# Kernel tuning notes

Measured on AMD Instinct MI355X. Metric: run time of the kernel, lower is better.

The kernel has to match this reference:

```python
import jax, jax.numpy as jnp
import numpy as np

B, N, PLANE, H, W = 2, 6, 64, 48, 48
HIDP = 64
PS = 3
RATES = 3


def conv2d(x, w, b, pad, dil=1):
    # x: [BN, Cin, H, W], w: [Cout, Cin, kh, kw]
    out = jax.lax.conv_general_dilated(
        x, w, window_strides=(1, 1),
        padding=[(pad, pad), (pad, pad)],
        rhs_dilation=(dil, dil),
        dimension_numbers=('NCHW', 'OIHW', 'NCHW'))
    return out + b[None, :, None, None]


def avgpool3(x):
    bn, c, h, w = x.shape
    return x.reshape(bn, c, h // PS, PS, w // PS, PS).mean(axis=(3, 5))


def setup_inputs() -> dict:
    key = jax.random.key(0)
    ks = jax.random.split(key, 20)
    s = 0.05
    hid_pa = PLANE * 3  # 192, hidden width of MultiFieldConv2d
    d = {
        'x': jax.random.normal(ks[0], (B, N, PLANE, H, W), jnp.float32),
        # patch_aggr: 3 dilated convs (rates 1..3), k=3, plane -> plane*3
        'pa_w1': jax.random.normal(ks[1], (hid_pa, PLANE, 3, 3)) * s,
        'pa_b1': jnp.zeros((hid_pa,)),
        'pa_w2': jax.random.normal(ks[2], (hid_pa, PLANE, 3, 3)) * s,
        'pa_b2': jnp.zeros((hid_pa,)),
        'pa_w3': jax.random.normal(ks[3], (hid_pa, PLANE, 3, 3)) * s,
        'pa_b3': jnp.zeros((hid_pa,)),
        # convert: 1x1 (hid_pa*rates -> 3*hidp), relu, 1x1 (3*hidp -> 3*hidp)
        'pa_cw1': jax.random.normal(ks[4], (3 * HIDP, hid_pa * RATES, 1, 1)) * s,
        'pa_cb1': jnp.zeros((3 * HIDP,)),
        'pa_cw2': jax.random.normal(ks[5], (3 * HIDP, 3 * HIDP, 1, 1)) * s,
        'pa_cb2': jnp.zeros((3 * HIDP,)),
        # to_kv conv: k=3 pad=1, hidp -> hidp
        'kv_w': jax.random.normal(ks[6], (HIDP, HIDP, 3, 3)) * s,
        'kv_b': jnp.zeros((HIDP,)),
        # to_out: 1x1 hidp->plane, relu, 1x1 plane->plane, relu
        'out_w1': jax.random.normal(ks[7], (PLANE, HIDP, 1, 1)) * s,
        'out_b1': jnp.zeros((PLANE,)),
        'out_w2': jax.random.normal(ks[8], (PLANE, PLANE, 1, 1)) * s,
        'out_b2': jnp.zeros((PLANE,)),
        'scales': jnp.ones((N,)),
    }
    return d


def reference(x, pa_w1, pa_b1, pa_w2, pa_b2, pa_w3, pa_b3,
              pa_cw1, pa_cb1, pa_cw2, pa_cb2,
              kv_w, kv_b, out_w1, out_b1, out_w2, out_b2, scales):
    b, n, c, h, w = x.shape
    scale = HIDP ** (-0.5)
    xf = x.reshape(b * n, c, h, w)

    # MultiFieldConv2d: dilated convs (same spatial size for odd k), concat, 1x1 convert
    u = jnp.concatenate([
        conv2d(xf, pa_w1, pa_b1, pad=1, dil=1),
        conv2d(xf, pa_w2, pa_b2, pad=2, dil=2),
        conv2d(xf, pa_w3, pa_b3, pad=3, dil=3),
    ], axis=1)
    qkv = conv2d(jax.nn.relu(conv2d(u, pa_cw1, pa_cb1, 0)), pa_cw2, pa_cb2, 0)
    qkv = jax.nn.relu(qkv)  # F.relu(patch_aggr(x))
    xq, xk, xv = jnp.split(qkv, 3, axis=1)  # each [BN, hidp, H, W]

    def to_kv(t):
        return avgpool3(jax.nn.relu(conv2d(t, kv_w, kv_b, pad=PS // 2)))

    k_ = to_kv(xk)                       # [BN, hidp, H/3, W/3]
    v_ = to_kv(xv) * (1.0 / PS ** 2)

    hw_kv = k_.shape[2] * k_.shape[3]
    Qs = xq.reshape(b, n, HIDP, h * w).transpose(0, 1, 3, 2)   # b n g d
    Ks = k_.reshape(b, n, HIDP, hw_kv).transpose(0, 1, 3, 2)   # b m k d
    Vs = v_.reshape(b, n, HIDP, hw_kv).transpose(0, 1, 3, 2)

    # Leave-one-out sigmoid attention: sum_{j != i} sigmoid(q_i k_j^T * scale) @ v_j
    # Computed as full sum minus the self (j == i) term (exact same math).
    A_all = jax.nn.sigmoid(jnp.einsum('bngd,bmkd->bngmk', Qs, Ks) * scale)
    out_all = jnp.einsum('bngmk,bmkd->bngd', A_all, Vs)
    A_self = jax.nn.sigmoid(jnp.einsum('bngd,bnkd->bngk', Qs, Ks) * scale)
    out_self = jnp.einsum('bngk,bnkd->bngd', A_self, Vs)
    attn_out = out_all - out_self                               # [b, n, HW, hidp]

    res = attn_out.transpose(0, 1, 3, 2).reshape(b, n, HIDP, h, w)
    xv5 = xv.reshape(b, n, HIDP, h, w)
    res = jax.nn.relu(res + scales[None, :, None, None, None] * xv5)

    rf = res.reshape(b * n, HIDP, h, w)
    o = jax.nn.relu(conv2d(jax.nn.relu(conv2d(rf, out_w1, out_b1, 0)), out_w2, out_b2, 0))
    return o.reshape(b, n, c, h, w)
```

## Files before the change

kernel.cpp:

```cpp
#include <hip/hip_runtime.h>
#include <hip/hip_bf16.h>
#include <math.h>

#define BB 2
#define NVIEW 6
#define BN 12
#define CIN 64
#define HH 48
#define WW 48
#define PP (HH*WW)
#define OC 192
#define HPA 192
#define HIDP 64
#define KHW 16
#define PK 256
#define PADW 54
#define PADA (PADW*PADW)
#define NTOT (BN*PP)
#define K1 1728
#define KVPW 50
#define KVPA (KVPW*KVPW)

typedef __attribute__((ext_vector_type(8))) short bf16x8;
typedef __attribute__((ext_vector_type(4))) float f32x4;

#define OFF_WEFFB 0
#define SZ_WEFFB_FL (OC*K1/2)
#define OFF_BEFF (OFF_WEFFB + SZ_WEFFB_FL)
#define SZ_BEFF 256
#define OFF_CW2B (OFF_BEFF + SZ_BEFF)
#define SZ_CW2B_FL (OC*OC/2)
#define OFF_WKVB (OFF_CW2B + SZ_CW2B_FL)
#define SZ_WKVB_FL (64*576/2)
#define OFF_PADXT (OFF_WKVB + SZ_WKVB_FL)
#define SZ_PADXT_FL (BN*PADA*64/2)
#define OFF_QB16 (OFF_PADXT + SZ_PADXT_FL)
#define SZ_QB16_FL (BN*PP*64/2)
#define OFF_KB16 (OFF_QB16 + SZ_QB16_FL)
#define SZ_KB16_FL (BN*PK*64/2)
#define OFF_VB16T (OFF_KB16 + SZ_KB16_FL)
#define SZ_VB16T_FL (BN*64*PK/2)
#define OFF_KVPAD (OFF_VB16T + SZ_VB16T_FL)
#define SZ_KVPAD_FL (BN*2*KVPA*64/2)
#define OFF_CONVB (OFF_KVPAD + SZ_KVPAD_FL)
#define SZ_CONVB_FL (BN*2*PP*64/2)
#define OFF_W1SW (OFF_CONVB + SZ_CONVB_FL)
#define SZ_WSW_FL 2048
#define OFF_W2SW (OFF_W1SW + SZ_WSW_FL)
#define OFF_ATTNP (OFF_W2SW + SZ_WSW_FL)
#define SZ_ATTNP (BN*PP*HIDP)
#define OFF_XVB16 (OFF_ATTNP + 2*SZ_ATTNP)
#define SZ_XVB16_FL (BN*PP*64/2)

__device__ __forceinline__ void load_lds16(const void* g, void* l) {
    __builtin_amdgcn_global_load_lds(
        (const __attribute__((address_space(1))) unsigned int*)g,
        (__attribute__((address_space(3))) unsigned int*)l, 16, 0, 0);
}

__device__ __forceinline__ unsigned short f2bu(float f) {
    __hip_bfloat16 h = __float2bfloat16(f);
    return *(unsigned short*)&h;
}

__device__ __forceinline__ float bu2f(unsigned short h) {
    unsigned int u = ((unsigned int)h) << 16;
    return *(float*)&u;
}

__global__ __launch_bounds__(192) void k_fold(const float* __restrict__ cw1,
                       const float* __restrict__ cb1,
                       const float* __restrict__ w1, const float* __restrict__ b1,
                       const float* __restrict__ w2, const float* __restrict__ b2,
                       const float* __restrict__ w3, const float* __restrict__ b3,
                       __hip_bfloat16* __restrict__ weffb, float* __restrict__ beff) {
    __shared__ float cw1s[8][HPA];
    int b = blockIdx.x;
    int r = b / 72;
    int rem = b % 72;
    int og = rem / 3, tz = rem % 3;
    int tid = threadIdx.x;
    int tg = tz*192 + tid;
    int ic = tg / 9, tap = tg % 9;
    const float* w = (r==0) ? w1 : (r==1) ? w2 : w3;
    #pragma unroll
    for (int j = 0; j < 8; ++j)
        cw1s[j][tid] = cw1[(size_t)(og*8+j)*(HPA*3) + r*HPA + tid];
    __syncthreads();
    float acc[8] = {0,0,0,0,0,0,0,0};
    for (int c = 0; c < HPA; ++c) {
        float wv = w[(size_t)c*(CIN*9) + tg];
        #pragma unroll
        for (int j = 0; j < 8; ++j)
            acc[j] += cw1s[j][c] * wv;
    }
    #pragma unroll
    for (int j = 0; j < 8; ++j)
        weffb[(size_t)(og*8+j)*K1 + r*576 + tap*64 + ic] = __float2bfloat16(acc[j]);
    if (r == 0 && tz == 0 && tid < 8) {
        int o = og*8 + tid;
        float bacc = cb1[o];
        for (int rr = 0; rr < 3; ++rr) {
            const float* bb = (rr==0)?b1:(rr==1)?b2:b3;
            for (int c = 0; c < HPA; ++c)
                bacc += cw1[(size_t)o*(HPA*3) + rr*HPA + c] * bb[c];
        }
        beff[o] = bacc;
    }
}

__global__ void k_wprep(const float* __restrict__ kvw, const float* __restrict__ cw2,
                        const float* __restrict__ w1, const float* __restrict__ w2,
                        __hip_bfloat16* __restrict__ wkvb, __hip_bfloat16* __restrict__ cw2b,
                        __hip_bfloat16* __restrict__ w1sw, __hip_bfloat16* __restrict__ w2sw) {
    int idx = blockIdx.x*256 + threadIdx.x;
    if (idx < 36864) {
        int oc = idx / 576, rest = idx % 576;
        int tap = rest / 64, ic = rest % 64;
        wkvb[idx] = __float2bfloat16(kvw[(oc*64 + ic)*9 + tap]);
    } else if (idx < 73728) {
        int i = idx - 36864;
        cw2b[i] = __float2bfloat16(cw2[i]);
    } else if (idx < 81920) {
        int i = idx - 73728;
        const float* w = (i < 4096) ? w1 : w2;
        __hip_bfloat16* dst = (i < 4096) ? w1sw : w2sw;
        int j = i & 4095;
        int oc = j >> 6, s = (j >> 3) & 7, e = j & 7;
        int k = ((s ^ (oc & 7)) << 3) + e;
        dst[j] = __float2bfloat16(w[oc*64 + k]);
    }
}

__global__ void k_padxT(const float* __restrict__ x, __hip_bfloat16* __restrict__ padxT) {
    int idx = blockIdx.x*256 + threadIdx.x;
    if (idx >= BN*PADA) return;
    int spos = idx % PADA; int bn = idx / PADA;
    int sy = spos / PADW, sx = spos % PADW;
    __hip_bfloat16* dst = padxT + (size_t)idx*64;
    if (sy >= 3 && sy < 51 && sx >= 3 && sx < 51) {
        const float* src = x + (size_t)bn*CIN*PP + (sy-3)*WW + (sx-3);
        #pragma unroll 8
        for (int ic = 0; ic < 64; ++ic) dst[ic] = __float2bfloat16(src[ic*PP]);
    } else {
        #pragma unroll 8
        for (int ic = 0; ic < 64; ++ic) dst[ic] = __float2bfloat16(0.f);
    }
}

__global__ void k_halo(__hip_bfloat16* __restrict__ kvpad) {
    int idx = blockIdx.x*256 + threadIdx.x;
    if (idx >= 24*196) return;
    int bn2 = idx / 196, h = idx % 196;
    int py, px;
    if (h < 50)       { py = 0;        px = h; }
    else if (h < 100) { py = 49;       px = h - 50; }
    else if (h < 148) { py = h - 99;   px = 0; }
    else              { py = h - 147;  px = 49; }
    bf16x8 z = (bf16x8){0,0,0,0,0,0,0,0};
    __hip_bfloat16* dst = kvpad + ((size_t)bn2*KVPA + py*KVPW + px)*64;
    #pragma unroll
    for (int j = 0; j < 8; ++j) *(bf16x8*)(dst + j*8) = z;
}

__global__ __launch_bounds__(256) void k_mfc(const __hip_bfloat16* __restrict__ wA,
        const __hip_bfloat16* __restrict__ pxT, const __hip_bfloat16* __restrict__ cw2b,
        const float* __restrict__ beff, const float* __restrict__ cb2,
        __hip_bfloat16* __restrict__ xvb16, __hip_bfloat16* __restrict__ qb16,
        __hip_bfloat16* __restrict__ kvpad) {
    __shared__ __align__(16) char smem[41472];
    int tid = threadIdx.x;
    int wid = tid >> 6, lane = tid & 63;
    int bn = blockIdx.x / 36;
    int pb = (blockIdx.x % 36) * 64;
    int sgr = ((lane&7) ^ (lane>>3)) * 8;
    int l7 = lane & 7, lh = lane >> 4, rrow = lane & 15, gcol = lane >> 4;

    size_t gbase[8];
    #pragma unroll
    for (int s2 = 0; s2 < 8; ++s2) {
        int seg = wid*8 + s2;
        if (seg < 24) {
            int row = seg*8 + (lane>>3);
            gbase[s2] = (size_t)row*K1 + sgr;
        } else {
            int p = pb + (seg-24)*8 + (lane>>3);
            int py = p / WW, px = p % WW;
            gbase[s2] = ((size_t)bn*PADA + (py+3)*PADW + (px+3))*64 + sgr;
        }
    }

    f32x4 acc1[3][4];
    #pragma unroll
    for (int m = 0; m < 3; ++m)
        #pragma unroll
        for (int nf = 0; nf < 4; ++nf) acc1[m][nf] = (f32x4){0.f,0.f,0.f,0.f};

    for (int kt = 0; kt < 27; ++kt) {
        int r_ = kt / 9, tap = kt - r_*9;
        int doff = (r_+1)*((tap/3 - 1)*PADW + (tap%3 - 1));
        __syncthreads();
        #pragma unroll
        for (int s2 = 0; s2 < 8; ++s2) {
            int seg = wid*8 + s2;
            const __hip_bfloat16* g = (seg < 24) ? wA + gbase[s2] + kt*64
                                                 : pxT + gbase[s2] + (size_t)doff*64;
            load_lds16(g, smem + seg*1024);
        }
        __syncthreads();
        bf16x8 a[3][2], b[4][2];
        #pragma unroll
        for (int kk = 0; kk < 2; ++kk) {
            int gof = ((kk*4 + lh) ^ l7) << 4;
            #pragma unroll
            for (int m = 0; m < 3; ++m)
                a[m][kk] = *(const bf16x8*)(smem + (wid*48 + m*16 + rrow)*128 + gof);
            #pragma unroll
            for (int nf = 0; nf < 4; ++nf)
                b[nf][kk] = *(const bf16x8*)(smem + 24576 + (nf*16 + rrow)*128 + gof);
        }
        #pragma unroll
        for (int kk = 0; kk < 2; ++kk)
            #pragma unroll
            for (int m = 0; m < 3; ++m)
                #pragma unroll
                for (int nf = 0; nf < 4; ++nf)
                    acc1[m][nf] = __builtin_amdgcn_mfma_f32_16x16x32_bf16(
                        a[m][kk], b[nf][kk], acc1[m][nf], 0, 0, 0);
    }

    f32x4 acc2[3][4];
    #pragma unroll
    for (int m = 0; m < 3; ++m)
        #pragma unroll
        for (int nf = 0; nf < 4; ++nf) acc2[m][nf] = (f32x4){0.f,0.f,0.f,0.f};

    for (int kt2 = 0; kt2 < 3; ++kt2) {
        __syncthreads();
        #pragma unroll
        for (int s2 = 0; s2 < 6; ++s2) {
            int seg = wid*6 + s2;
            int row = seg*8 + (lane>>3);
            load_lds16(cw2b + (size_t)row*OC + kt2*64 + sgr, smem + seg*1024);
        }
        #pragma unroll
        for (int m = 0; m < 3; ++m) {
            int oc16 = wid*48 + m*16;
            if ((oc16 >> 6) == kt2) {
                int oc0 = oc16 + gcol*4;
                float4 bz = *(const float4*)&beff[oc0];
                int cb = (oc0 - kt2*64)*2;
                #pragma unroll
                for (int nf = 0; nf < 4; ++nf) {
                    int px = nf*16 + rrow;
                    ushort4 hv;
                    hv.x = f2bu(fmaxf(acc1[m][nf][0] + bz.x, 0.f));
                    hv.y = f2bu(fmaxf(acc1[m][nf][1] + bz.y, 0.f));
                    hv.z = f2bu(fmaxf(acc1[m][nf][2] + bz.z, 0.f));
                    hv.w = f2bu(fmaxf(acc1[m][nf][3] + bz.w, 0.f));
                    *(ushort4*)(smem + 32768 + px*136 + cb) = hv;
                }
            }
        }
        __syncthreads();
        #pragma unroll
        for (int kk = 0; kk < 2; ++kk) {
            int gofA = ((kk*4 + lh) ^ l7) << 4;
            int gofB = (kk*4 + lh) << 4;
            bf16x8 a2[3], b2[4];
            #pragma unroll
            for (int m2 = 0; m2 < 3; ++m2)
                a2[m2] = *(const bf16x8*)(smem + (wid*48 + m2*16 + rrow)*128 + gofA);
            #pragma unroll
            for (int nf = 0; nf < 4; ++nf)
                b2[nf] = *(const bf16x8*)(smem + 32768 + (nf*16 + rrow)*136 + gofB);
            #pragma unroll
            for (int m2 = 0; m2 < 3; ++m2)
                #pragma unroll
                for (int nf = 0; nf < 4; ++nf)
                    acc2[m2][nf] = __builtin_amdgcn_mfma_f32_16x16x32_bf16(
                        a2[m2], b2[nf], acc2[m2][nf], 0, 0, 0);
        }
    }

    #pragma unroll
    for (int m2 = 0; m2 < 3; ++m2) {
        int oc16 = wid*48 + m2*16;
        int sec = oc16 >> 6;
        int oc0 = oc16 + gcol*4;
        float4 cz = *(const float4*)&cb2[oc0];
        #pragma unroll
        for (int nf = 0; nf < 4; ++nf) {
            int px = nf*16 + rrow;
            int p = pb + px;
            ushort4 bv;
            bv.x = f2bu(fmaxf(acc2[m2][nf][0] + cz.x, 0.f));
            bv.y = f2bu(fmaxf(acc2[m2][nf][1] + cz.y, 0.f));
            bv.z = f2bu(fmaxf(acc2[m2][nf][2] + cz.z, 0.f));
            bv.w = f2bu(fmaxf(acc2[m2][nf][3] + cz.w, 0.f));
            if (sec == 0) {
                *(ushort4*)&qb16[((size_t)bn*PP + p)*64 + oc0] = bv;
            } else {
                int kv = sec - 1;
                int py = p / WW, pxx = p % WW;
                int d = oc0 - (sec << 6);
                *(ushort4*)&kvpad[((size_t)(bn*2+kv)*KVPA + (py+1)*KVPW + pxx+1)*64 + d] = bv;
                if (kv == 1)
                    *(ushort4*)&xvb16[((size_t)bn*PP + p)*64 + d] = bv;
            }
        }
    }
}

__global__ __launch_bounds__(256) void k_kvgemm(const __hip_bfloat16* __restrict__ wA,
        const __hip_bfloat16* __restrict__ kvpad, const float* __restrict__ kvb,
        __hip_bfloat16* __restrict__ convb) {
    __shared__ __align__(16) char smem[24576];
    int tid = threadIdx.x;
    int wid = tid >> 6, lane = tid & 63;
    int tileN = blockIdx.x * 128;
    int bn2 = tileN / PP, p0 = tileN % PP;
    int sgr = ((lane&7) ^ (lane>>3)) * 8;

    size_t gbase[6];
    #pragma unroll
    for (int s2 = 0; s2 < 6; ++s2) {
        int seg = wid*6 + s2;
        if (seg < 8) {
            int row = seg*8 + (lane>>3);
            gbase[s2] = (size_t)row*576 + sgr;
        } else {
            int p = p0 + (seg-8)*8 + (lane>>3);
            int py = p / WW, px = p % WW;
            gbase[s2] = ((size_t)bn2*KVPA + (py+1)*KVPW + px+1)*64 + sgr;
        }
    }
    int wr = wid >> 1, wc = wid & 1;
    int l7 = lane & 7, lh = lane >> 4;
    int arowb[2], browb[4];
    #pragma unroll
    for (int m = 0; m < 2; ++m)
        arowb[m] = (wr*32 + m*16 + (lane&15))*128;
    #pragma unroll
    for (int nf = 0; nf < 4; ++nf)
        browb[nf] = 8192 + (wc*64 + nf*16 + (lane&15))*128;

    f32x4 acc[2][4];
    #pragma unroll
    for (int m = 0; m < 2; ++m)
        #pragma unroll
        for (int nf = 0; nf < 4; ++nf) acc[m][nf] = (f32x4){0.f,0.f,0.f,0.f};

    for (int kt = 0; kt < 9; ++kt) {
        int dy = kt/3 - 1, dx = kt%3 - 1;
        int doff = dy*KVPW + dx;
        __syncthreads();
        #pragma unroll
        for (int s2 = 0; s2 < 6; ++s2) {
            int seg = wid*6 + s2;
            const __hip_bfloat16* g = (seg < 8) ? wA + gbase[s2] + kt*64
                                                : kvpad + gbase[s2] + (size_t)doff*64;
            load_lds16(g, smem + seg*1024);
        }
        __syncthreads();
        bf16x8 a[2][2], b[4][2];
        #pragma unroll
        for (int kk = 0; kk < 2; ++kk) {
            int gof = ((kk*4 + lh) ^ l7) << 4;
            #pragma unroll
            for (int m = 0; m < 2; ++m)
                a[m][kk] = *(const bf16x8*)(smem + arowb[m] + gof);
            #pragma unroll
            for (int nf = 0; nf < 4; ++nf)
                b[nf][kk] = *(const bf16x8*)(smem + browb[nf] + gof);
        }
        #pragma unroll
        for (int kk = 0; kk < 2; ++kk)
            #pragma unroll
            for (int m = 0; m < 2; ++m)
                #pragma unroll
                for (int nf = 0; nf < 4; ++nf)
                    acc[m][nf] = __builtin_amdgcn_mfma_f32_16x16x32_bf16(
                        a[m][kk], b[nf][kk], acc[m][nf], 0, 0, 0);
    }
    #pragma unroll
    for (int m = 0; m < 2; ++m) {
        int rbase = wr*32 + m*16 + (lane>>4)*4;
        float4 bz = *(const float4*)&kvb[rbase];
        #pragma unroll
        for (int nf = 0; nf < 4; ++nf) {
            int col = p0 + wc*64 + nf*16 + (lane&15);
            ushort4 cv;
            cv.x = f2bu(fmaxf(acc[m][nf][0] + bz.x, 0.f));
            cv.y = f2bu(fmaxf(acc[m][nf][1] + bz.y, 0.f));
            cv.z = f2bu(fmaxf(acc[m][nf][2] + bz.z, 0.f));
            cv.w = f2bu(fmaxf(acc[m][nf][3] + bz.w, 0.f));
            *(ushort4*)&convb[((size_t)bn2*PP + col)*64 + rbase] = cv;
        }
    }
}

__global__ __launch_bounds__(256) void k_pool(const __hip_bfloat16* __restrict__ convb,
        __hip_bfloat16* __restrict__ kbufb, __hip_bfloat16* __restrict__ vbufT) {
    int idx = blockIdx.x*256 + threadIdx.x;
    int dg = idx % 8; idx /= 8;
    int pp = idx % PK; idx /= PK;
    int bn2 = idx;
    int kv = bn2 & 1, bn = bn2 >> 1;
    int qy = pp / KHW, qx = pp % KHW;
    float s[8] = {0,0,0,0,0,0,0,0};
    const __hip_bfloat16* base = convb + (size_t)bn2*PP*64 + dg*8;
    #pragma unroll
    for (int sy = 0; sy < 3; ++sy)
        #pragma unroll
        for (int sx = 0; sx < 3; ++sx) {
            union { bf16x8 v; unsigned short h[8]; } c;
            c.v = *(const bf16x8*)(base + ((size_t)(qy*3+sy)*WW + qx*3+sx)*64);
            #pragma unroll
            for (int j = 0; j < 8; ++j) s[j] += bu2f(c.h[j]);
        }
    if (kv == 0) {
        union { ushort4 u[2]; unsigned short h[8]; } cv;
        #pragma unroll
        for (int j = 0; j < 8; ++j) cv.h[j] = f2bu(s[j] * (1.f/9.f));
        ushort4* dst = (ushort4*)(kbufb + ((size_t)bn*PK + pp)*64 + dg*8);
        dst[0] = cv.u[0]; dst[1] = cv.u[1];
    } else {
        #pragma unroll
        for (int j = 0; j < 8; ++j)
            vbufT[((size_t)bn*64 + dg*8 + j)*PK + pp] = __float2bfloat16(s[j]*(1.f/81.f));
    }
}

__global__ __launch_bounds__(256) void k_attn3(const __hip_bfloat16* __restrict__ qb16,
        const __hip_bfloat16* __restrict__ kbufb, const __hip_bfloat16* __restrict__ vbufT,
        float* __restrict__ attnp) {
    __shared__ __align__(16) char smem[32768];
    char* Qs = smem;
    char* Ks = smem + 8192;
    char* Vs = smem + 16384;
    char* Ps = smem + 24576;
    int tid = threadIdx.x;
    int wid = tid >> 6, lane = tid & 63;
    int bid = blockIdx.x;
    int ks = bid & 1; bid >>= 1;
    int qt = bid % 36; int bn = bid / 36;
    int b = bn / NVIEW, n = bn % NVIEW;
    int p0 = qt*64;

    {
        const char* gq = (const char*)(qb16 + ((size_t)bn*PP + p0)*64);
        #pragma unroll
        for (int i = 0; i < 2; ++i) {
            int s = wid*2 + i;
            int lin = s*1024 + lane*16;
            int r = lin >> 7, c = (lin >> 4) & 7;
            int gof = (r<<7) + ((c ^ (r&7)) << 4);
            load_lds16(gq + gof, Qs + s*1024);
        }
    }
    int arow = wid*16 + (lane&15);
    int brow = lane&15;
    int gcol = lane>>4;
    int vrow = tid >> 2;
    int vc2 = (tid & 3) * 2;

    f32x4 oacc[4];
    #pragma unroll
    for (int i = 0; i < 4; ++i) oacc[i] = (f32x4){0,0,0,0};

    for (int mi = 0; mi < NVIEW-1; ++mi) {
        int m = mi + (mi >= n ? 1 : 0);
        int bnk = b*NVIEW + m;
        const char* gk = (const char*)(kbufb + (size_t)bnk*PK*64);
        const __hip_bfloat16* gv = vbufT + (size_t)bnk*64*PK;
        for (int kc = ks*2; kc < ks*2+2; ++kc) {
            __syncthreads();
            #pragma unroll
            for (int i = 0; i < 2; ++i) {
                int s = wid*2 + i;
                int lin = s*1024 + lane*16;
                int r = lin >> 7, c = (lin >> 4) & 7;
                int gof = (r<<7) + ((c ^ (r&7)) << 4);
                load_lds16(gk + (size_t)kc*8192 + gof, Ks + s*1024);
            }
            {
                const __hip_bfloat16* src = gv + vrow*PK + kc*64 + vc2*8;
                bf16x8 v0 = *(const bf16x8*)src;
                bf16x8 v1 = *(const bf16x8*)(src+8);
                *(bf16x8*)(Vs + vrow*128 + ((vc2 ^ (vrow&7))<<4)) = v0;
                *(bf16x8*)(Vs + vrow*128 + (((vc2+1) ^ (vrow&7))<<4)) = v1;
            }
            __syncthreads();
            f32x4 sacc[4];
            #pragma unroll
            for (int i = 0; i < 4; ++i) sacc[i] = (f32x4){0,0,0,0};
            #pragma unroll
            for (int kk = 0; kk < 2; ++kk) {
                int g = kk*4 + gcol;
                bf16x8 af = *(const bf16x8*)(Ks + arow*128 + ((g ^ (arow&7))<<4));
                #pragma unroll
                for (int nf = 0; nf < 4; ++nf) {
                    int q = nf*16 + brow;
                    bf16x8 bq = *(const bf16x8*)(Qs + q*128 + ((g ^ (q&7))<<4));
                    sacc[nf] = __builtin_amdgcn_mfma_f32_16x16x32_bf16(af, bq, sacc[nf], 0,0,0);
                }
            }
            {
                int kbase = wid*16 + gcol*4;
                #pragma unroll
                for (int nf = 0; nf < 4; ++nf) {
                    int q = nf*16 + brow;
                    ushort4 pu;
                    float e0 = __expf(-sacc[nf][0]*0.125f);
                    float e1 = __expf(-sacc[nf][1]*0.125f);
                    float e2 = __expf(-sacc[nf][2]*0.125f);
                    float e3 = __expf(-sacc[nf][3]*0.125f);
                    pu.x = f2bu(__builtin_amdgcn_rcpf(1.f+e0));
                    pu.y = f2bu(__builtin_amdgcn_rcpf(1.f+e1));
                    pu.z = f2bu(__builtin_amdgcn_rcpf(1.f+e2));
                    pu.w = f2bu(__builtin_amdgcn_rcpf(1.f+e3));
                    *(ushort4*)(Ps + q*128 + (((kbase>>3) ^ (q&7))<<4) + (kbase&7)*2) = pu;
                }
            }
            __syncthreads();
            #pragma unroll
            for (int kk = 0; kk < 2; ++kk) {
                int g = kk*4 + gcol;
                int qr = wid*16 + brow;
                bf16x8 pf = *(const bf16x8*)(Ps + qr*128 + ((g ^ (qr&7))<<4));
                #pragma unroll
                for (int nf = 0; nf < 4; ++nf) {
                    int d = nf*16 + brow;
                    bf16x8 vf = *(const bf16x8*)(Vs + d*128 + ((g ^ (d&7))<<4));
                    oacc[nf] = __builtin_amdgcn_mfma_f32_16x16x32_bf16(pf, vf, oacc[nf], 0,0,0);
                }
            }
        }
    }
    float* ab = attnp + (size_t)ks*SZ_ATTNP + ((size_t)bn*PP + p0)*64;
    #pragma unroll
    for (int nf = 0; nf < 4; ++nf) {
        #pragma unroll
        for (int r = 0; r < 4; ++r) {
            int q = wid*16 + gcol*4 + r;
            int d = nf*16 + brow;
            ab[(size_t)q*64 + d] = oacc[nf][r];
        }
    }
}

__global__ __launch_bounds__(256) void k_out2(const float* __restrict__ attnp,
        const __hip_bfloat16* __restrict__ xvb16, const float* __restrict__ scales,
        const __hip_bfloat16* __restrict__ w1sw, const __hip_bfloat16* __restrict__ w2sw,
        const float* __restrict__ b1, const float* __restrict__ b2,
        float* __restrict__ out) {
    __shared__ __align__(16) char smem[49152];
    char* W1s = smem;
    char* W2s = smem + 8192;
    char* Rs  = smem + 16384;
    char* Ts  = smem + 32768;
    int tid = threadIdx.x;
    int wid = tid >> 6, lane = tid & 63;
    int pix0 = blockIdx.x * 128;
    int bn = pix0 / PP;
    int pb = pix0 - bn*PP;
    float sc = scales[bn % NVIEW];

    #pragma unroll
    for (int i = 0; i < 4; ++i) {
        int seg = wid*4 + i;
        const char* src = (seg < 8) ? (const char*)w1sw + seg*1024
                                    : (const char*)w2sw + (seg-8)*1024;
        load_lds16(src + lane*16, smem + seg*1024);
    }
    {
        int p = tid >> 1, d0 = (tid & 1) * 32;
        int P = pix0 + p;
        const float* a0 = attnp + (size_t)P*64 + d0;
        const float* a1 = a0 + SZ_ATTNP;
        const __hip_bfloat16* xv = xvb16 + (size_t)P*64 + d0;
        #pragma unroll
        for (int j = 0; j < 4; ++j) {
            float4 u0 = *(const float4*)(a0 + j*8);
            float4 u1 = *(const float4*)(a0 + j*8 + 4);
            float4 v0 = *(const float4*)(a1 + j*8);
            float4 v1 = *(const float4*)(a1 + j*8 + 4);
            union { bf16x8 v; unsigned short h[8]; } xu;
            xu.v = *(const bf16x8*)(xv + j*8);
            union { bf16x8 v; unsigned short h[8]; } rv;
            rv.h[0] = f2bu(fmaxf(u0.x + v0.x + sc*bu2f(xu.h[0]), 0.f));
            rv.h[1] = f2bu(fmaxf(u0.y + v0.y + sc*bu2f(xu.h[1]), 0.f));
            rv.h[2] = f2bu(fmaxf(u0.z + v0.z + sc*bu2f(xu.h[2]), 0.f));
            rv.h[3] = f2bu(fmaxf(u0.w + v0.w + sc*bu2f(xu.h[3]), 0.f));
            rv.h[4] = f2bu(fmaxf(u1.x + v1.x + sc*bu2f(xu.h[4]), 0.f));
            rv.h[5] = f2bu(fmaxf(u1.y + v1.y + sc*bu2f(xu.h[5]), 0.f));
            rv.h[6] = f2bu(fmaxf(u1.z + v1.z + sc*bu2f(xu.h[6]), 0.f));
            rv.h[7] = f2bu(fmaxf(u1.w + v1.w + sc*bu2f(xu.h[7]), 0.f));
            int g = (d0 >> 3) + j;
            *(bf16x8*)(Rs + p*128 + ((g ^ (p&7)) << 4)) = rv.v;
        }
    }
    __syncthreads();

    int wr = wid >> 1, wc = wid & 1;
    int rrow = lane & 15, gcol = lane >> 4;
    f32x4 acc1[2][4];
    #pragma unroll
    for (int m = 0; m < 2; ++m)
        #pragma unroll
        for (int nf = 0; nf < 4; ++nf) acc1[m][nf] = (f32x4){0,0,0,0};
    #pragma unroll
    for (int kk = 0; kk < 2; ++kk) {
        int g = kk*4 + gcol;
        #pragma unroll
        for (int m = 0; m < 2; ++m) {
            int oc = wr*32 + m*16 + rrow;
            bf16x8 af = *(const bf16x8*)(W1s + oc*128 + ((g ^ (oc&7)) << 4));
            #pragma unroll
            for (int nf = 0; nf < 4; ++nf) {
                int px = wc*64 + nf*16 + rrow;
                bf16x8 bf = *(const bf16x8*)(Rs + px*128 + ((g ^ (px&7)) << 4));
                acc1[m][nf] = __builtin_amdgcn_mfma_f32_16x16x32_bf16(af, bf, acc1[m][nf], 0,0,0);
            }
        }
    }
    #pragma unroll
    for (int m = 0; m < 2; ++m) {
        int oc0 = wr*32 + m*16 + gcol*4;
        float4 bz = *(const float4*)&b1[oc0];
        #pragma unroll
        for (int nf = 0; nf < 4; ++nf) {
            int px = wc*64 + nf*16 + rrow;
            ushort4 tv;
            tv.x = f2bu(fmaxf(acc1[m][nf][0] + bz.x, 0.f));
            tv.y = f2bu(fmaxf(acc1[m][nf][1] + bz.y, 0.f));
            tv.z = f2bu(fmaxf(acc1[m][nf][2] + bz.z, 0.f));
            tv.w = f2bu(fmaxf(acc1[m][nf][3] + bz.w, 0.f));
            *(ushort4*)(Ts + px*128 + (((oc0>>3) ^ (px&7)) << 4) + (oc0&7)*2) = tv;
        }
    }
    __syncthreads();
    f32x4 acc2[2][4];
    #pragma unroll
    for (int m = 0; m < 2; ++m)
        #pragma unroll
        for (int nf = 0; nf < 4; ++nf) acc2[m][nf] = (f32x4){0,0,0,0};
    #pragma unroll
    for (int kk = 0; kk < 2; ++kk) {
        int g = kk*4 + gcol;
        #pragma unroll
        for (int m = 0; m < 2; ++m) {
            int oc = wr*32 + m*16 + rrow;
            bf16x8 af = *(const bf16x8*)(W2s + oc*128 + ((g ^ (oc&7)) << 4));
            #pragma unroll
            for (int nf = 0; nf < 4; ++nf) {
                int px = wc*64 + nf*16 + rrow;
                bf16x8 bf = *(const bf16x8*)(Ts + px*128 + ((g ^ (px&7)) << 4));
                acc2[m][nf] = __builtin_amdgcn_mfma_f32_16x16x32_bf16(af, bf, acc2[m][nf], 0,0,0);
            }
        }
    }
    #pragma unroll
    for (int m = 0; m < 2; ++m) {
        int oc0 = wr*32 + m*16 + gcol*4;
        float4 bz = *(const float4*)&b2[oc0];
        #pragma unroll
        for (int nf = 0; nf < 4; ++nf) {
            int px = wc*64 + nf*16 + rrow;
            float* dst = out + ((size_t)bn*64 + oc0)*PP + pb + px;
            dst[0*PP] = fmaxf(acc2[m][nf][0] + bz.x, 0.f);
            dst[1*PP] = fmaxf(acc2[m][nf][1] + bz.y, 0.f);
            dst[2*PP] = fmaxf(acc2[m][nf][2] + bz.z, 0.f);
            dst[3*PP] = fmaxf(acc2[m][nf][3] + bz.w, 0.f);
        }
    }
}

extern "C" void kernel_launch(void* const* d_in, const int* in_sizes, int n_in,
                              void* d_out, int out_size, void* d_ws, size_t ws_size,
                              hipStream_t stream) {
    (void)in_sizes; (void)n_in; (void)out_size; (void)ws_size;
    const float* x      = (const float*)d_in[0];
    const float* pa_w1  = (const float*)d_in[1];
    const float* pa_b1  = (const float*)d_in[2];
    const float* pa_w2  = (const float*)d_in[3];
    const float* pa_b2  = (const float*)d_in[4];
    const float* pa_w3  = (const float*)d_in[5];
    const float* pa_b3  = (const float*)d_in[6];
    const float* pa_cw1 = (const float*)d_in[7];
    const float* pa_cb1 = (const float*)d_in[8];
    const float* pa_cw2 = (const float*)d_in[9];
    const float* pa_cb2 = (const float*)d_in[10];
    const float* kv_w   = (const float*)d_in[11];
    const float* kv_b   = (const float*)d_in[12];
    const float* out_w1 = (const float*)d_in[13];
    const float* out_b1 = (const float*)d_in[14];
    const float* out_w2 = (const float*)d_in[15];
    const float* out_b2 = (const float*)d_in[16];
    const float* scales = (const float*)d_in[17];
    float* out = (float*)d_out;
    float* ws  = (float*)d_ws;

    __hip_bfloat16* weffb = (__hip_bfloat16*)(ws + OFF_WEFFB);
    float* beff = ws + OFF_BEFF;
    __hip_bfloat16* cw2b  = (__hip_bfloat16*)(ws + OFF_CW2B);
    __hip_bfloat16* wkvb  = (__hip_bfloat16*)(ws + OFF_WKVB);
    __hip_bfloat16* padxT = (__hip_bfloat16*)(ws + OFF_PADXT);
    __hip_bfloat16* qb16  = (__hip_bfloat16*)(ws + OFF_QB16);
    __hip_bfloat16* kbufb = (__hip_bfloat16*)(ws + OFF_KB16);
    __hip_bfloat16* vbufT = (__hip_bfloat16*)(ws + OFF_VB16T);
    __hip_bfloat16* kvpad = (__hip_bfloat16*)(ws + OFF_KVPAD);
    __hip_bfloat16* convb = (__hip_bfloat16*)(ws + OFF_CONVB);
    __hip_bfloat16* w1sw  = (__hip_bfloat16*)(ws + OFF_W1SW);
    __hip_bfloat16* w2sw  = (__hip_bfloat16*)(ws + OFF_W2SW);
    float* attnp = ws + OFF_ATTNP;
    __hip_bfloat16* xvb16 = (__hip_bfloat16*)(ws + OFF_XVB16);

    k_fold<<<216, 192, 0, stream>>>(pa_cw1, pa_cb1, pa_w1, pa_b1,
                                    pa_w2, pa_b2, pa_w3, pa_b3, weffb, beff);
    k_wprep<<<320, 256, 0, stream>>>(kv_w, pa_cw2, out_w1, out_w2,
                                     wkvb, cw2b, w1sw, w2sw);
    k_padxT<<<(BN*PADA+255)/256, 256, 0, stream>>>(x, padxT);
    k_halo<<<(24*196+255)/256, 256, 0, stream>>>(kvpad);
    k_mfc<<<NTOT/64, 256, 0, stream>>>(weffb, padxT, cw2b, beff, pa_cb2,
                                       xvb16, qb16, kvpad);
    k_kvgemm<<<BN*2*PP/128, 256, 0, stream>>>(wkvb, kvpad, kv_b, convb);
    k_pool<<<BN*2*PK*8/256, 256, 0, stream>>>(convb, kbufb, vbufT);
    k_attn3<<<BN*36*2, 256, 0, stream>>>(qb16, kbufb, vbufT, attnp);
    k_out2<<<NTOT/128, 256, 0, stream>>>(attnp, xvb16, scales, w1sw, w2sw,
                                         out_b1, out_b2, out);
}
```

Before: 123.3 us.

## Double-buffer LDS in conv GEMM kernels and fold halo zeroing into weight prep

The k_mfc and k_kvgemm main loops now use two LDS buffers: the next K-tile's global-to-LDS loads are issued before the current tile's MFMAs, and each iteration needs one barrier instead of two. This is meant to hide global load latency behind compute. The kvpad halo-zeroing kernel is merged into k_wprep, which removes one launch. The LDS footprint grows (k_mfc to 64KB, k_kvgemm to 48KB), which may cut the number of blocks resident per CU.

```diff
diff --git a/kernel.cpp b/kernel.cpp
--- a/kernel.cpp
+++ b/kernel.cpp
@@ -112,7 +112,8 @@
 __global__ void k_wprep(const float* __restrict__ kvw, const float* __restrict__ cw2,
                         const float* __restrict__ w1, const float* __restrict__ w2,
                         __hip_bfloat16* __restrict__ wkvb, __hip_bfloat16* __restrict__ cw2b,
-                        __hip_bfloat16* __restrict__ w1sw, __hip_bfloat16* __restrict__ w2sw) {
+                        __hip_bfloat16* __restrict__ w1sw, __hip_bfloat16* __restrict__ w2sw,
+                        __hip_bfloat16* __restrict__ kvpad) {
     int idx = blockIdx.x*256 + threadIdx.x;
     if (idx < 36864) {
         int oc = idx / 576, rest = idx % 576;
@@ -129,6 +130,18 @@
         int oc = j >> 6, s = (j >> 3) & 7, e = j & 7;
         int k = ((s ^ (oc & 7)) << 3) + e;
         dst[j] = __float2bfloat16(w[oc*64 + k]);
+    } else if (idx < 86624) {
+        int i = idx - 81920;
+        int bn2 = i / 196, h = i % 196;
+        int py, px;
+        if (h < 50)       { py = 0;        px = h; }
+        else if (h < 100) { py = 49;       px = h - 50; }
+        else if (h < 148) { py = h - 99;   px = 0; }
+        else              { py = h - 147;  px = 49; }
+        bf16x8 z = (bf16x8){0,0,0,0,0,0,0,0};
+        __hip_bfloat16* dst = kvpad + ((size_t)bn2*KVPA + py*KVPW + px)*64;
+        #pragma unroll
+        for (int j = 0; j < 8; ++j) *(bf16x8*)(dst + j*8) = z;
     }
 }
 
@@ -148,27 +161,12 @@
     }
 }
 
-__global__ void k_halo(__hip_bfloat16* __restrict__ kvpad) {
-    int idx = blockIdx.x*256 + threadIdx.x;
-    if (idx >= 24*196) return;
-    int bn2 = idx / 196, h = idx % 196;
-    int py, px;
-    if (h < 50)       { py = 0;        px = h; }
-    else if (h < 100) { py = 49;       px = h - 50; }
-    else if (h < 148) { py = h - 99;   px = 0; }
-    else              { py = h - 147;  px = 49; }
-    bf16x8 z = (bf16x8){0,0,0,0,0,0,0,0};
-    __hip_bfloat16* dst = kvpad + ((size_t)bn2*KVPA + py*KVPW + px)*64;
-    #pragma unroll
-    for (int j = 0; j < 8; ++j) *(bf16x8*)(dst + j*8) = z;
-}
-
 __global__ __launch_bounds__(256) void k_mfc(const __hip_bfloat16* __restrict__ wA,
         const __hip_bfloat16* __restrict__ pxT, const __hip_bfloat16* __restrict__ cw2b,
         const float* __restrict__ beff, const float* __restrict__ cb2,
         __hip_bfloat16* __restrict__ xvb16, __hip_bfloat16* __restrict__ qb16,
         __hip_bfloat16* __restrict__ kvpad) {
-    __shared__ __align__(16) char smem[41472];
+    __shared__ __align__(16) char smem[65536];
     int tid = threadIdx.x;
     int wid = tid >> 6, lane = tid & 63;
     int bn = blockIdx.x / 36;
@@ -177,47 +175,59 @@
     int l7 = lane & 7, lh = lane >> 4, rrow = lane & 15, gcol = lane >> 4;
 
     size_t gbase[8];
+    int dbase[8];
     #pragma unroll
     for (int s2 = 0; s2 < 8; ++s2) {
         int seg = wid*8 + s2;
         if (seg < 24) {
             int row = seg*8 + (lane>>3);
             gbase[s2] = (size_t)row*K1 + sgr;
+            dbase[s2] = seg*1024;
         } else {
             int p = pb + (seg-24)*8 + (lane>>3);
             int py = p / WW, px = p % WW;
             gbase[s2] = ((size_t)bn*PADA + (py+3)*PADW + (px+3))*64 + sgr;
-        }
-    }
-
-    f32x4 acc1[3][4];
-    #pragma unroll
-    for (int m = 0; m < 3; ++m)
-        #pragma unroll
-        for (int nf = 0; nf < 4; ++nf) acc1[m][nf] = (f32x4){0.f,0.f,0.f,0.f};
-
-    for (int kt = 0; kt < 27; ++kt) {
+            dbase[s2] = 49152 + (seg-24)*1024;
+        }
+    }
+
+    auto stage1 = [&](int kt, int par) {
         int r_ = kt / 9, tap = kt - r_*9;
         int doff = (r_+1)*((tap/3 - 1)*PADW + (tap%3 - 1));
-        __syncthreads();
+        int poA = par ? 24576 : 0;
+        int poB = par ? 8192 : 0;
         #pragma unroll
         for (int s2 = 0; s2 < 8; ++s2) {
             int seg = wid*8 + s2;
             const __hip_bfloat16* g = (seg < 24) ? wA + gbase[s2] + kt*64
                                                  : pxT + gbase[s2] + (size_t)doff*64;
-            load_lds16(g, smem + seg*1024);
-        }
-        __syncthreads();
+            load_lds16(g, smem + dbase[s2] + ((seg < 24) ? poA : poB));
+        }
+    };
+
+    f32x4 acc1[3][4];
+    #pragma unroll
+    for (int m = 0; m < 3; ++m)
+        #pragma unroll
+        for (int nf = 0; nf < 4; ++nf) acc1[m][nf] = (f32x4){0.f,0.f,0.f,0.f};
+
+    stage1(0, 0);
+    __syncthreads();
+    for (int kt = 0; kt < 27; ++kt) {
+        int par = kt & 1;
+        if (kt < 26) stage1(kt+1, par^1);
+        int aB = par ? 24576 : 0;
+        int bB = 49152 + (par ? 8192 : 0);
         bf16x8 a[3][2], b[4][2];
         #pragma unroll
         for (int kk = 0; kk < 2; ++kk) {
             int gof = ((kk*4 + lh) ^ l7) << 4;
             #pragma unroll
             for (int m = 0; m < 3; ++m)
-                a[m][kk] = *(const bf16x8*)(smem + (wid*48 + m*16 + rrow)*128 + gof);
+                a[m][kk] = *(const bf16x8*)(smem + aB + (wid*48 + m*16 + rrow)*128 + gof);
             #pragma unroll
             for (int nf = 0; nf < 4; ++nf)
-                b[nf][kk] = *(const bf16x8*)(smem + 24576 + (nf*16 + rrow)*128 + gof);
+                b[nf][kk] = *(const bf16x8*)(smem + bB + (nf*16 + rrow)*128 + gof);
         }
         #pragma unroll
         for (int kk = 0; kk < 2; ++kk)
@@ -227,6 +237,7 @@
                 for (int nf = 0; nf < 4; ++nf)
                     acc1[m][nf] = __builtin_amdgcn_mfma_f32_16x16x32_bf16(
                         a[m][kk], b[nf][kk], acc1[m][nf], 0, 0, 0);
+        __syncthreads();
     }
 
     f32x4 acc2[3][4];
@@ -236,7 +247,7 @@
         for (int nf = 0; nf < 4; ++nf) acc2[m][nf] = (f32x4){0.f,0.f,0.f,0.f};
 
     for (int kt2 = 0; kt2 < 3; ++kt2) {
-        __syncthreads();
+        if (kt2) __syncthreads();
         #pragma unroll
         for (int s2 = 0; s2 < 6; ++s2) {
             int seg = wid*6 + s2;
@@ -258,7 +269,7 @@
                     hv.y = f2bu(fmaxf(acc1[m][nf][1] + bz.y, 0.f));
                     hv.z = f2bu(fmaxf(acc1[m][nf][2] + bz.z, 0.f));
                     hv.w = f2bu(fmaxf(acc1[m][nf][3] + bz.w, 0.f));
-                    *(ushort4*)(smem + 32768 + px*136 + cb) = hv;
+                    *(ushort4*)(smem + 49152 + px*136 + cb) = hv;
                 }
             }
         }
@@ -273,7 +284,7 @@
                 a2[m2] = *(const bf16x8*)(smem + (wid*48 + m2*16 + rrow)*128 + gofA);
             #pragma unroll
             for (int nf = 0; nf < 4; ++nf)
-                b2[nf] = *(const bf16x8*)(smem + 32768 + (nf*16 + rrow)*136 + gofB);
+                b2[nf] = *(const bf16x8*)(smem + 49152 + (nf*16 + rrow)*136 + gofB);
             #pragma unroll
             for (int m2 = 0; m2 < 3; ++m2)
                 #pragma unroll
@@ -315,7 +326,7 @@
 __global__ __launch_bounds__(256) void k_kvgemm(const __hip_bfloat16* __restrict__ wA,
         const __hip_bfloat16* __restrict__ kvpad, const float* __restrict__ kvb,
         __hip_bfloat16* __restrict__ convb) {
-    __shared__ __align__(16) char smem[24576];
+    __shared__ __align__(16) char smem[49152];
     int tid = threadIdx.x;
     int wid = tid >> 6, lane = tid & 63;
     int tileN = blockIdx.x * 128;
@@ -335,44 +346,49 @@
             gbase[s2] = ((size_t)bn2*KVPA + (py+1)*KVPW + px+1)*64 + sgr;
         }
     }
-    int wr = wid >> 1, wc = wid & 1;
-    int l7 = lane & 7, lh = lane >> 4;
-    int arowb[2], browb[4];
-    #pragma unroll
-    for (int m = 0; m < 2; ++m)
-        arowb[m] = (wr*32 + m*16 + (lane&15))*128;
-    #pragma unroll
-    for (int nf = 0; nf < 4; ++nf)
-        browb[nf] = 8192 + (wc*64 + nf*16 + (lane&15))*128;
-
-    f32x4 acc[2][4];
-    #pragma unroll
-    for (int m = 0; m < 2; ++m)
-        #pragma unroll
-        for (int nf = 0; nf < 4; ++nf) acc[m][nf] = (f32x4){0.f,0.f,0.f,0.f};
-
-    for (int kt = 0; kt < 9; ++kt) {
+    auto stage2 = [&](int kt, int par) {
         int dy = kt/3 - 1, dx = kt%3 - 1;
         int doff = dy*KVPW + dx;
-        __syncthreads();
         #pragma unroll
         for (int s2 = 0; s2 < 6; ++s2) {
             int seg = wid*6 + s2;
             const __hip_bfloat16* g = (seg < 8) ? wA + gbase[s2] + kt*64
                                                 : kvpad + gbase[s2] + (size_t)doff*64;
-            load_lds16(g, smem + seg*1024);
-        }
-        __syncthreads();
+            load_lds16(g, smem + par*24576 + seg*1024);
+        }
+    };
+    int wr = wid >> 1, wc = wid & 1;
+    int l7 = lane & 7, lh = lane >> 4;
+    int arowb[2], browb[4];
+    #pragma unroll
+    for (int m = 0; m < 2; ++m)
+        arowb[m] = (wr*32 + m*16 + (lane&15))*128;
+    #pragma unroll
+    for (int nf = 0; nf < 4; ++nf)
+        browb[nf] = 8192 + (wc*64 + nf*16 + (lane&15))*128;
+
+    f32x4 acc[2][4];
+    #pragma unroll
+    for (int m = 0; m < 2; ++m)
+        #pragma unroll
+        for (int nf = 0; nf < 4; ++nf) acc[m][nf] = (f32x4){0.f,0.f,0.f,0.f};
+
+    stage2(0, 0);
+    __syncthreads();
+    for (int kt = 0; kt < 9; ++kt) {
+        int par = kt & 1;
+        if (kt < 8) stage2(kt+1, par^1);
+        int po = par*24576;
         bf16x8 a[2][2], b[4][2];
         #pragma unroll
         for (int kk = 0; kk < 2; ++kk) {
             int gof = ((kk*4 + lh) ^ l7) << 4;
             #pragma unroll
             for (int m = 0; m < 2; ++m)
-                a[m][kk] = *(const bf16x8*)(smem + arowb[m] + gof);
+                a[m][kk] = *(const bf16x8*)(smem + po + arowb[m] + gof);
             #pragma unroll
             for (int nf = 0; nf < 4; ++nf)
-                b[nf][kk] = *(const bf16x8*)(smem + browb[nf] + gof);
+                b[nf][kk] = *(const bf16x8*)(smem + po + browb[nf] + gof);
         }
         #pragma unroll
         for (int kk = 0; kk < 2; ++kk)
@@ -382,6 +398,7 @@
                 for (int nf = 0; nf < 4; ++nf)
                     acc[m][nf] = __builtin_amdgcn_mfma_f32_16x16x32_bf16(
                         a[m][kk], b[nf][kk], acc[m][nf], 0, 0, 0);
+        __syncthreads();
     }
     #pragma unroll
     for (int m = 0; m < 2; ++m) {
@@ -719,10 +736,9 @@
 
     k_fold<<<216, 192, 0, stream>>>(pa_cw1, pa_cb1, pa_w1, pa_b1,
                                     pa_w2, pa_b2, pa_w3, pa_b3, weffb, beff);
-    k_wprep<<<320, 256, 0, stream>>>(kv_w, pa_cw2, out_w1, out_w2,
-                                     wkvb, cw2b, w1sw, w2sw);
+    k_wprep<<<339, 256, 0, stream>>>(kv_w, pa_cw2, out_w1, out_w2,
+                                     wkvb, cw2b, w1sw, w2sw, kvpad);
     k_padxT<<<(BN*PADA+255)/256, 256, 0, stream>>>(x, padxT);
-    k_halo<<<(24*196+255)/256, 256, 0, stream>>>(kvpad);
     k_mfc<<<NTOT/64, 256, 0, stream>>>(weffb, padxT, cw2b, beff, pa_cb2,
                                        xvb16, qb16, kvpad);
     k_kvgemm<<<BN*2*PP/128, 256, 0, stream>>>(wkvb, kvpad, kv_b, convb);
```

Measured after the change: 113.5 us. -7.9%, faster.
